# Kernel tuning notes

Hardware: AMD Instinct MI355X
Metric: run time of the kernel (lower is better)

The kernel has to match this reference:

```python
import jax, jax.numpy as jnp
import numpy as np

NUM_SEG = 4096
N = 1048576
H = 256

def setup_inputs() -> dict:
    key = jax.random.key(0)
    kx, kb, kei, ket, kw1, kb1, kw2, kb2 = jax.random.split(key, 8)
    x = jax.random.normal(kx, (N, H), dtype=jnp.float32)
    batch = jnp.sort(jax.random.randint(kb, (N,), 0, NUM_SEG))
    edge_index = jax.random.randint(kei, (2, 4096), 0, N)
    edge_type = jax.random.randint(ket, (4096,), 0, 4)
    s1 = 1.0 / np.sqrt(H)
    W1 = jax.random.uniform(kw1, (H, H), jnp.float32, -s1, s1)
    b1 = jax.random.uniform(kb1, (H,), jnp.float32, -s1, s1)
    W2 = jax.random.uniform(kw2, (H, H), jnp.float32, -s1, s1)
    b2 = jax.random.uniform(kb2, (H,), jnp.float32, -s1, s1)
    return {"x": x, "edge_index": edge_index, "edge_type": edge_type,
            "batch": batch, "W1": W1, "b1": b1, "W2": W2, "b2": b2}

def reference(x, edge_index, edge_type, batch, W1, b1, W2, b2):
    # Fused segment-mean over all rows (replaces the Python per-group loop).
    sums = jax.ops.segment_sum(x, batch, num_segments=NUM_SEG)        # [S, H]
    cnt = jax.ops.segment_sum(jnp.ones((x.shape[0],), x.dtype), batch,
                              num_segments=NUM_SEG)                    # [S]
    pooled = sums / jnp.maximum(cnt, 1.0)[:, None]                     # [S, H]
    # 2-layer MLP: Linear -> exact GELU -> (Dropout=identity in eval) -> Linear
    h = jax.nn.gelu(pooled @ W1 + b1, approximate=False)
    return h @ W2 + b2
```

## Files before the change

### kernel.cpp

```cpp
#include <hip/hip_runtime.h>
#include <math.h>

#define NSEG 4096
#define HDIM 256
#define SPB  16

typedef float f32x4 __attribute__((ext_vector_type(4)));

__device__ __forceinline__ float gelu_exact(float z) {
    return 0.5f * z * (1.0f + erff(z * 0.7071067811865476f));
}

__global__ __launch_bounds__(256)
void seg_offsets_kernel(const int* __restrict__ batch, int* __restrict__ offs, int N) {
    int i = blockIdx.x * 256 + threadIdx.x;
    if (i > NSEG) return;
    int lo = 0, hi = N;
    while (lo < hi) { int m = (lo + hi) >> 1; if (batch[m] < i) lo = m + 1; else hi = m; }
    offs[i] = lo;
}

__global__ __launch_bounds__(256)
void pool_kernel(const float* __restrict__ x, const int* __restrict__ offs,
                 float* __restrict__ pooled) {
    const int s    = blockIdx.x;
    const int tid  = threadIdx.x;
    const int wave = tid >> 6;
    const int lane = tid & 63;
    const int r0 = offs[s], r1 = offs[s + 1];
    const float* colp = x + (size_t)lane * 4;

    f32x4 acc[8];
    #pragma unroll
    for (int u = 0; u < 8; ++u) acc[u] = (f32x4)(0.f);

    int r = r0 + wave;
    for (; r + 28 < r1; r += 32) {
        #pragma unroll
        for (int u = 0; u < 8; ++u) {
            const f32x4 v = __builtin_nontemporal_load(
                reinterpret_cast<const f32x4*>(colp + (size_t)(r + 4 * u) * HDIM));
            acc[u] += v;
        }
    }
    for (; r < r1; r += 4) {
        const f32x4 v = __builtin_nontemporal_load(
            reinterpret_cast<const f32x4*>(colp + (size_t)r * HDIM));
        acc[0] += v;
    }
    #pragma unroll
    for (int u = 0; u < 4; ++u) acc[u] += acc[u + 4];
    acc[0] += acc[2];
    acc[1] += acc[3];
    acc[0] += acc[1];

    __shared__ float part[4][HDIM];
    *reinterpret_cast<f32x4*>(&part[wave][lane * 4]) = acc[0];
    __syncthreads();
    float sum = (part[0][tid] + part[1][tid]) + (part[2][tid] + part[3][tid]);
    const int cnt = r1 - r0;
    pooled[(size_t)s * HDIM + tid] = sum / (float)(cnt > 1 ? cnt : 1);
}

__global__ __launch_bounds__(256)
void mlp_kernel(const float* __restrict__ pooled,
                const float* __restrict__ W1, const float* __restrict__ b1,
                const float* __restrict__ W2, const float* __restrict__ b2,
                float* __restrict__ out) {
    const int s0   = blockIdx.x * SPB;
    const int tid  = threadIdx.x;
    const int row0 = (tid >> 6) * 4;
    const int col0 = (tid & 63) * 4;

    __shared__ float P[SPB][HDIM];
    __shared__ float Hs[SPB][HDIM];

    #pragma unroll
    for (int i = 0; i < SPB; ++i)
        P[i][tid] = pooled[(size_t)(s0 + i) * HDIM + tid];
    __syncthreads();

    float acc[4][4];
    #pragma unroll
    for (int i = 0; i < 4; ++i)
        #pragma unroll
        for (int j = 0; j < 4; ++j) acc[i][j] = 0.f;

    for (int k = 0; k < HDIM; k += 4) {
        const float4 w0 = *(const float4*)(W1 + (size_t)(k + 0) * HDIM + col0);
        const float4 w1 = *(const float4*)(W1 + (size_t)(k + 1) * HDIM + col0);
        const float4 w2 = *(const float4*)(W1 + (size_t)(k + 2) * HDIM + col0);
        const float4 w3 = *(const float4*)(W1 + (size_t)(k + 3) * HDIM + col0);
        #pragma unroll
        for (int i = 0; i < 4; ++i) {
            const float4 p = *(const float4*)(&P[row0 + i][k]);
            acc[i][0] = fmaf(p.x, w0.x, acc[i][0]); acc[i][1] = fmaf(p.x, w0.y, acc[i][1]);
            acc[i][2] = fmaf(p.x, w0.z, acc[i][2]); acc[i][3] = fmaf(p.x, w0.w, acc[i][3]);
            acc[i][0] = fmaf(p.y, w1.x, acc[i][0]); acc[i][1] = fmaf(p.y, w1.y, acc[i][1]);
            acc[i][2] = fmaf(p.y, w1.z, acc[i][2]); acc[i][3] = fmaf(p.y, w1.w, acc[i][3]);
            acc[i][0] = fmaf(p.z, w2.x, acc[i][0]); acc[i][1] = fmaf(p.z, w2.y, acc[i][1]);
            acc[i][2] = fmaf(p.z, w2.z, acc[i][2]); acc[i][3] = fmaf(p.z, w2.w, acc[i][3]);
            acc[i][0] = fmaf(p.w, w3.x, acc[i][0]); acc[i][1] = fmaf(p.w, w3.y, acc[i][1]);
            acc[i][2] = fmaf(p.w, w3.z, acc[i][2]); acc[i][3] = fmaf(p.w, w3.w, acc[i][3]);
        }
    }
    {
        const float4 bb = *(const float4*)(b1 + col0);
        const float bv[4] = {bb.x, bb.y, bb.z, bb.w};
        #pragma unroll
        for (int i = 0; i < 4; ++i) {
            float4 h;
            h.x = gelu_exact(acc[i][0] + bv[0]);
            h.y = gelu_exact(acc[i][1] + bv[1]);
            h.z = gelu_exact(acc[i][2] + bv[2]);
            h.w = gelu_exact(acc[i][3] + bv[3]);
            *(float4*)&Hs[row0 + i][col0] = h;
        }
    }
    __syncthreads();

    #pragma unroll
    for (int i = 0; i < 4; ++i)
        #pragma unroll
        for (int j = 0; j < 4; ++j) acc[i][j] = 0.f;

    for (int k = 0; k < HDIM; k += 4) {
        const float4 w0 = *(const float4*)(W2 + (size_t)(k + 0) * HDIM + col0);
        const float4 w1 = *(const float4*)(W2 + (size_t)(k + 1) * HDIM + col0);
        const float4 w2 = *(const float4*)(W2 + (size_t)(k + 2) * HDIM + col0);
        const float4 w3 = *(const float4*)(W2 + (size_t)(k + 3) * HDIM + col0);
        #pragma unroll
        for (int i = 0; i < 4; ++i) {
            const float4 p = *(const float4*)(&Hs[row0 + i][k]);
            acc[i][0] = fmaf(p.x, w0.x, acc[i][0]); acc[i][1] = fmaf(p.x, w0.y, acc[i][1]);
            acc[i][2] = fmaf(p.x, w0.z, acc[i][2]); acc[i][3] = fmaf(p.x, w0.w, acc[i][3]);
            acc[i][0] = fmaf(p.y, w1.x, acc[i][0]); acc[i][1] = fmaf(p.y, w1.y, acc[i][1]);
            acc[i][2] = fmaf(p.y, w1.z, acc[i][2]); acc[i][3] = fmaf(p.y, w1.w, acc[i][3]);
            acc[i][0] = fmaf(p.z, w2.x, acc[i][0]); acc[i][1] = fmaf(p.z, w2.y, acc[i][1]);
            acc[i][2] = fmaf(p.z, w2.z, acc[i][2]); acc[i][3] = fmaf(p.z, w2.w, acc[i][3]);
            acc[i][0] = fmaf(p.w, w3.x, acc[i][0]); acc[i][1] = fmaf(p.w, w3.y, acc[i][1]);
            acc[i][2] = fmaf(p.w, w3.z, acc[i][2]); acc[i][3] = fmaf(p.w, w3.w, acc[i][3]);
        }
    }
    {
        const float4 bb = *(const float4*)(b2 + col0);
        const float bv[4] = {bb.x, bb.y, bb.z, bb.w};
        #pragma unroll
        for (int i = 0; i < 4; ++i) {
            float4 o;
            o.x = acc[i][0] + bv[0];
            o.y = acc[i][1] + bv[1];
            o.z = acc[i][2] + bv[2];
            o.w = acc[i][3] + bv[3];
            *(float4*)(out + (size_t)(s0 + row0 + i) * HDIM + col0) = o;
        }
    }
}

__global__ __launch_bounds__(256)
void fused_pool_mlp(const float* __restrict__ x, const int* __restrict__ batch,
                    const float* __restrict__ W1, const float* __restrict__ b1,
                    const float* __restrict__ W2, const float* __restrict__ b2,
                    float* __restrict__ out, int N)
{
    const int s = blockIdx.x, tid = threadIdx.x;
    const int wave = tid >> 6, lane = tid & 63;
    __shared__ int s_r0, s_r1;
    if (tid == 0) {
        int lo = 0, hi = N;
        while (lo < hi) { int m = (lo + hi) >> 1; if (batch[m] < s)     lo = m + 1; else hi = m; }
        s_r0 = lo; hi = N;
        while (lo < hi) { int m = (lo + hi) >> 1; if (batch[m] < s + 1) lo = m + 1; else hi = m; }
        s_r1 = lo;
    }
    __syncthreads();
    const int r0 = s_r0, r1 = s_r1;
    float4 a0 = make_float4(0.f,0.f,0.f,0.f), a1 = a0;
    int r = r0 + wave;
    for (; r + 4 < r1; r += 8) {
        const float4 v0 = *(const float4*)(x + (size_t)r       * HDIM + lane * 4);
        const float4 v1 = *(const float4*)(x + (size_t)(r + 4) * HDIM + lane * 4);
        a0.x += v0.x; a0.y += v0.y; a0.z += v0.z; a0.w += v0.w;
        a1.x += v1.x; a1.y += v1.y; a1.z += v1.z; a1.w += v1.w;
    }
    if (r < r1) {
        const float4 v0 = *(const float4*)(x + (size_t)r * HDIM + lane * 4);
        a0.x += v0.x; a0.y += v0.y; a0.z += v0.z; a0.w += v0.w;
    }
    a0.x += a1.x; a0.y += a1.y; a0.z += a1.z; a0.w += a1.w;
    __shared__ float4 part4[4][64];
    __shared__ float pooled[HDIM];
    __shared__ float hbuf[HDIM];
    part4[wave][lane] = a0;
    __syncthreads();
    const float* pf = (const float*)part4;
    float sum = (pf[tid] + pf[256 + tid]) + (pf[512 + tid] + pf[768 + tid]);
    const int cnt = r1 - r0;
    pooled[tid] = sum / (float)(cnt > 1 ? cnt : 1);
    __syncthreads();
    float c0 = 0.f, c1 = 0.f, c2 = 0.f, c3 = 0.f;
    for (int k = 0; k < HDIM; k += 4) {
        c0 = fmaf(pooled[k + 0], W1[(k + 0) * HDIM + tid], c0);
        c1 = fmaf(pooled[k + 1], W1[(k + 1) * HDIM + tid], c1);
        c2 = fmaf(pooled[k + 2], W1[(k + 2) * HDIM + tid], c2);
        c3 = fmaf(pooled[k + 3], W1[(k + 3) * HDIM + tid], c3);
    }
    const float z = (c0 + c1) + (c2 + c3) + b1[tid];
    hbuf[tid] = gelu_exact(z);
    __syncthreads();
    c0 = c1 = c2 = c3 = 0.f;
    for (int k = 0; k < HDIM; k += 4) {
        c0 = fmaf(hbuf[k + 0], W2[(k + 0) * HDIM + tid], c0);
        c1 = fmaf(hbuf[k + 1], W2[(k + 1) * HDIM + tid], c1);
        c2 = fmaf(hbuf[k + 2], W2[(k + 2) * HDIM + tid], c2);
        c3 = fmaf(hbuf[k + 3], W2[(k + 3) * HDIM + tid], c3);
    }
    out[(size_t)s * HDIM + tid] = (c0 + c1) + (c2 + c3) + b2[tid];
}

extern "C" void kernel_launch(void* const* d_in, const int* in_sizes, int n_in,
                              void* d_out, int out_size, void* d_ws, size_t ws_size,
                              hipStream_t stream) {
    const float* x     = (const float*)d_in[0];
    const int*   batch = (const int*)  d_in[3];
    const float* W1    = (const float*)d_in[4];
    const float* b1    = (const float*)d_in[5];
    const float* W2    = (const float*)d_in[6];
    const float* b2    = (const float*)d_in[7];
    float* out = (float*)d_out;
    const int N = in_sizes[3];

    const size_t pooled_bytes = (size_t)NSEG * HDIM * sizeof(float);
    const size_t offs_bytes   = (size_t)(NSEG + 1) * sizeof(int);

    if (ws_size >= pooled_bytes + offs_bytes) {
        float* pooled = (float*)d_ws;
        int*   offs   = (int*)((char*)d_ws + pooled_bytes);
        hipLaunchKernelGGL(seg_offsets_kernel, dim3((NSEG + 256) / 256), dim3(256), 0, stream,
                           batch, offs, N);
        hipLaunchKernelGGL(pool_kernel, dim3(NSEG), dim3(256), 0, stream,
                           x, offs, pooled);
        hipLaunchKernelGGL(mlp_kernel, dim3(NSEG / SPB), dim3(256), 0, stream,
                           pooled, W1, b1, W2, b2, out);
    } else {
        hipLaunchKernelGGL(fused_pool_mlp, dim3(NSEG), dim3(256), 0, stream,
                           x, batch, W1, b1, W2, b2, out, N);
    }
}
```

Measured before the change: 201.3 us.

## Compute segment offsets by boundary scan and shrink MLP tile to eight segments

Segment offsets are now computed by a streaming scan over the sorted batch array. Each thread reads four ids and writes the offsets at each boundary it sees, replacing the per-segment binary searches. The MLP kernel processes 8 segments per block instead of 16, doubling the block count for better occupancy, and writes its output with nontemporal stores. The scan reads the full 4 MB batch array and adds a launch condition requiring N divisible by 4, and the grid size uses truncating division, which assumes N is a multiple of 1024.

```diff
diff --git a/kernel.cpp b/kernel.cpp
--- a/kernel.cpp
+++ b/kernel.cpp
@@ -3,9 +3,10 @@
 
 #define NSEG 4096
 #define HDIM 256
-#define SPB  16
+#define SPB  8
 
 typedef float f32x4 __attribute__((ext_vector_type(4)));
+typedef int   i32x4 __attribute__((ext_vector_type(4)));
 
 __device__ __forceinline__ float gelu_exact(float z) {
     return 0.5f * z * (1.0f + erff(z * 0.7071067811865476f));
@@ -13,11 +14,21 @@
 
 __global__ __launch_bounds__(256)
 void seg_offsets_kernel(const int* __restrict__ batch, int* __restrict__ offs, int N) {
-    int i = blockIdx.x * 256 + threadIdx.x;
-    if (i > NSEG) return;
-    int lo = 0, hi = N;
-    while (lo < hi) { int m = (lo + hi) >> 1; if (batch[m] < i) lo = m + 1; else hi = m; }
-    offs[i] = lo;
+    const int t = blockIdx.x * 256 + threadIdx.x;
+    const int j = t * 4;
+    if (j >= N) return;
+    const i32x4 v = __builtin_nontemporal_load(reinterpret_cast<const i32x4*>(batch + j));
+    const int prev = (t == 0) ? -1 : batch[j - 1];
+    int a = prev;
+    #pragma unroll
+    for (int u = 0; u < 4; ++u) {
+        const int b_ = v[u];
+        for (int b = a + 1; b <= b_; ++b) offs[b] = j + u;
+        a = b_;
+    }
+    if (j + 3 == N - 1) {
+        for (int b = a + 1; b <= NSEG; ++b) offs[b] = N;
+    }
 }
 
 __global__ __launch_bounds__(256)
@@ -69,7 +80,7 @@
                 float* __restrict__ out) {
     const int s0   = blockIdx.x * SPB;
     const int tid  = threadIdx.x;
-    const int row0 = (tid >> 6) * 4;
+    const int row0 = (tid >> 6) * 2;
     const int col0 = (tid & 63) * 4;
 
     __shared__ float P[SPB][HDIM];
@@ -80,9 +91,9 @@
         P[i][tid] = pooled[(size_t)(s0 + i) * HDIM + tid];
     __syncthreads();
 
-    float acc[4][4];
-    #pragma unroll
-    for (int i = 0; i < 4; ++i)
+    float acc[2][4];
+    #pragma unroll
+    for (int i = 0; i < 2; ++i)
         #pragma unroll
         for (int j = 0; j < 4; ++j) acc[i][j] = 0.f;
 
@@ -92,7 +103,7 @@
         const float4 w2 = *(const float4*)(W1 + (size_t)(k + 2) * HDIM + col0);
         const float4 w3 = *(const float4*)(W1 + (size_t)(k + 3) * HDIM + col0);
         #pragma unroll
-        for (int i = 0; i < 4; ++i) {
+        for (int i = 0; i < 2; ++i) {
             const float4 p = *(const float4*)(&P[row0 + i][k]);
             acc[i][0] = fmaf(p.x, w0.x, acc[i][0]); acc[i][1] = fmaf(p.x, w0.y, acc[i][1]);
             acc[i][2] = fmaf(p.x, w0.z, acc[i][2]); acc[i][3] = fmaf(p.x, w0.w, acc[i][3]);
@@ -108,7 +119,7 @@
         const float4 bb = *(const float4*)(b1 + col0);
         const float bv[4] = {bb.x, bb.y, bb.z, bb.w};
         #pragma unroll
-        for (int i = 0; i < 4; ++i) {
+        for (int i = 0; i < 2; ++i) {
             float4 h;
             h.x = gelu_exact(acc[i][0] + bv[0]);
             h.y = gelu_exact(acc[i][1] + bv[1]);
@@ -120,7 +131,7 @@
     __syncthreads();
 
     #pragma unroll
-    for (int i = 0; i < 4; ++i)
+    for (int i = 0; i < 2; ++i)
         #pragma unroll
         for (int j = 0; j < 4; ++j) acc[i][j] = 0.f;
 
@@ -130,7 +141,7 @@
         const float4 w2 = *(const float4*)(W2 + (size_t)(k + 2) * HDIM + col0);
         const float4 w3 = *(const float4*)(W2 + (size_t)(k + 3) * HDIM + col0);
         #pragma unroll
-        for (int i = 0; i < 4; ++i) {
+        for (int i = 0; i < 2; ++i) {
             const float4 p = *(const float4*)(&Hs[row0 + i][k]);
             acc[i][0] = fmaf(p.x, w0.x, acc[i][0]); acc[i][1] = fmaf(p.x, w0.y, acc[i][1]);
             acc[i][2] = fmaf(p.x, w0.z, acc[i][2]); acc[i][3] = fmaf(p.x, w0.w, acc[i][3]);
@@ -144,15 +155,15 @@
     }
     {
         const float4 bb = *(const float4*)(b2 + col0);
-        const float bv[4] = {bb.x, bb.y, bb.z, bb.w};
-        #pragma unroll
-        for (int i = 0; i < 4; ++i) {
-            float4 o;
-            o.x = acc[i][0] + bv[0];
-            o.y = acc[i][1] + bv[1];
-            o.z = acc[i][2] + bv[2];
-            o.w = acc[i][3] + bv[3];
-            *(float4*)(out + (size_t)(s0 + row0 + i) * HDIM + col0) = o;
+        #pragma unroll
+        for (int i = 0; i < 2; ++i) {
+            f32x4 o;
+            o.x = acc[i][0] + bb.x;
+            o.y = acc[i][1] + bb.y;
+            o.z = acc[i][2] + bb.z;
+            o.w = acc[i][3] + bb.w;
+            __builtin_nontemporal_store(o,
+                reinterpret_cast<f32x4*>(out + (size_t)(s0 + row0 + i) * HDIM + col0));
         }
     }
 }
@@ -233,10 +244,10 @@
     const size_t pooled_bytes = (size_t)NSEG * HDIM * sizeof(float);
     const size_t offs_bytes   = (size_t)(NSEG + 1) * sizeof(int);
 
-    if (ws_size >= pooled_bytes + offs_bytes) {
+    if (ws_size >= pooled_bytes + offs_bytes && (N & 3) == 0) {
         float* pooled = (float*)d_ws;
         int*   offs   = (int*)((char*)d_ws + pooled_bytes);
-        hipLaunchKernelGGL(seg_offsets_kernel, dim3((NSEG + 256) / 256), dim3(256), 0, stream,
+        hipLaunchKernelGGL(seg_offsets_kernel, dim3(N / 4 / 256), dim3(256), 0, stream,
                            batch, offs, N);
         hipLaunchKernelGGL(pool_kernel, dim3(NSEG), dim3(256), 0, stream,
                            x, offs, pooled);
```

Result: slower. 209.8 us (+4.2%).
